# Kernel optimization log

Hardware: AMD Instinct MI355X
Metric: run time of the kernel (lower is better)

The kernel has to match this reference:

```python
import jax, jax.numpy as jnp
import numpy as np

B, DIN, N = 4096, 1024, 1024

def _hard_sigmoid(z):
    # Keras hard_sigmoid: clip(0.2*x + 0.5, 0, 1)
    return jnp.clip(0.2 * z + 0.5, 0.0, 1.0)

def setup_inputs() -> dict:
    key = jax.random.key(0)
    ks = jax.random.split(key, 12)
    s_in = 1.0 / np.sqrt(DIN)
    s_h = 1.0 / np.sqrt(N)
    d = {
        'x': jax.random.normal(ks[0], (B, DIN), jnp.float32),
        'c0': jax.random.normal(ks[1], (B, N), jnp.float32),
        'h0': jax.random.normal(ks[2], (B, N), jnp.float32),
        'Wf': jax.random.normal(ks[3], (DIN, N), jnp.float32) * s_in,
        'Wi': jax.random.normal(ks[4], (DIN, N), jnp.float32) * s_in,
        'Wo': jax.random.normal(ks[5], (DIN, N), jnp.float32) * s_in,
        'Wc': jax.random.normal(ks[6], (DIN, N), jnp.float32) * s_in,
        'Uf': jax.random.normal(ks[7], (N, N), jnp.float32) * s_h,
        'Ui': jax.random.normal(ks[8], (N, N), jnp.float32) * s_h,
        'Uo': jax.random.normal(ks[9], (N, N), jnp.float32) * s_h,
        'Uc': jax.random.normal(ks[10], (N, N), jnp.float32) * s_h,
        'bf': jnp.zeros((N,), jnp.float32),
        'bi': jnp.zeros((N,), jnp.float32),
        'bo': jnp.zeros((N,), jnp.float32),
        'bc': jnp.zeros((N,), jnp.float32),
    }
    return d

def reference(x, c0, h0, Wf, Wi, Wo, Wc, Uf, Ui, Uo, Uc, bf, bi, bo, bc):
    # Fuse the 8 small Dense ops into two GEMMs on concatenated weights
    W = jnp.concatenate([Wf, Wi, Wo, Wc], axis=1)            # [DIN, 4N]
    U = jnp.concatenate([Uf, Ui, Uo, Uc], axis=1)            # [N, 4N]
    b = jnp.concatenate([bf, bi, bo, bc], axis=0)            # [4N]
    z = x @ W + h0 @ U + b                                   # [B, 4N]
    zf, zi, zo, zc = jnp.split(z, 4, axis=1)
    f = _hard_sigmoid(zf)
    i = _hard_sigmoid(zi)
    o = _hard_sigmoid(zo)
    c_tilde = jnp.tanh(zc)
    c = f * c0 + i * c_tilde
    h = o * jnp.tanh(c)
    return (h, c, h)  # (output, new_c, new_h)
```

## Files before the change

kernel.cpp:

```cpp
#include <hip/hip_runtime.h>
#include <hip/hip_bf16.h>
#include <stdint.h>

typedef unsigned short u16;
typedef __attribute__((ext_vector_type(8))) short short8;
typedef __attribute__((ext_vector_type(4))) float f32x4;

#define BATCH 4096
#define DIN   1024
#define NH    1024
#define KTOT  2048
#define BM    128
#define BN    32
#define BK    64

__device__ __forceinline__ void gload_lds16(const void* gp, void* lp) {
    __builtin_amdgcn_global_load_lds(
        (const __attribute__((address_space(1))) uint32_t*)gp,
        (__attribute__((address_space(3))) uint32_t*)lp, 16, 0, 0);
}

__device__ __forceinline__ u16 f2bf(float f) {
    uint32_t t; __builtin_memcpy(&t, &f, 4);
    uint32_t r = (t + 0x7FFFu + ((t >> 16) & 1u)) >> 16;
    return (u16)r;
}
__device__ __forceinline__ float hsig(float z) {
    return fminf(fmaxf(fmaf(z, 0.2f, 0.5f), 0.0f), 1.0f);
}
__device__ __forceinline__ float fast_tanh(float x) {
    x = fminf(fmaxf(x, -12.0f), 12.0f);
    float e = __expf(2.0f * x);
    return (e - 1.0f) / (e + 1.0f);
}

#define WT_BLOCKS 2048
__global__ __launch_bounds__(256) void prep_kernel(
    const float* __restrict__ x, const float* __restrict__ h0,
    const float* __restrict__ Wf, const float* __restrict__ Wi,
    const float* __restrict__ Wo, const float* __restrict__ Wc,
    const float* __restrict__ Uf, const float* __restrict__ Ui,
    const float* __restrict__ Uo, const float* __restrict__ Uc,
    u16* __restrict__ Bt, u16* __restrict__ Abuf)
{
    __shared__ u16 tile[64][65];
    const int bid = blockIdx.x;
    const int tid = threadIdx.x;

    if (bid < WT_BLOCKS) {
        const int mz = bid >> 8;
        const float* srcs[8] = {Wf, Wi, Wo, Wc, Uf, Ui, Uo, Uc};
        const float* src = srcs[mz];
        const int g    = mz & 3;
        const int koff = (mz >> 2) << 10;
        const int k0 = ((bid >> 4) & 15) * 64;
        const int n0 = (bid & 15) * 64;

#pragma unroll
        for (int i = 0; i < 4; i++) {
            int idx = i * 256 + tid;
            int kk = idx >> 4, c = idx & 15;
            float4 v = *(const float4*)(src + (size_t)(k0 + kk) * NH + n0 + c * 4);
            u16* dst = &tile[kk][c * 4];
            dst[0] = f2bf(v.x); dst[1] = f2bf(v.y);
            dst[2] = f2bf(v.z); dst[3] = f2bf(v.w);
        }
        __syncthreads();
#pragma unroll
        for (int i = 0; i < 2; i++) {
            int idx = i * 256 + tid;
            int nn = idx >> 3, c = idx & 7;
            union { u16 v[8]; uint4 q; } pk;
#pragma unroll
            for (int j = 0; j < 8; j++) pk.v[j] = tile[c * 8 + j][nn];
            *(uint4*)(Bt + ((size_t)(g * NH + n0 + nn)) * KTOT + koff + k0 + c * 8) = pk.q;
        }
    } else {
        const int c  = (bid - WT_BLOCKS) * 256 + tid;
        const int m  = c >> 8;
        const int kc = (c & 255) * 8;
        const float* src = (kc < DIN) ? (x + (size_t)m * DIN + kc)
                                      : (h0 + (size_t)m * DIN + (kc - DIN));
        float4 v0 = *(const float4*)(src);
        float4 v1 = *(const float4*)(src + 4);
        union { u16 v[8]; uint4 q; } pk;
        pk.v[0] = f2bf(v0.x); pk.v[1] = f2bf(v0.y);
        pk.v[2] = f2bf(v0.z); pk.v[3] = f2bf(v0.w);
        pk.v[4] = f2bf(v1.x); pk.v[5] = f2bf(v1.y);
        pk.v[6] = f2bf(v1.z); pk.v[7] = f2bf(v1.w);
        *(uint4*)(Abuf + (size_t)m * KTOT + kc) = pk.q;
    }
}

__global__ __launch_bounds__(256, 2) void lstm_gemm_kernel(
    const u16* __restrict__ Abuf, const float* __restrict__ c0,
    const u16* __restrict__ Bt,
    const float* __restrict__ bfv, const float* __restrict__ biv,
    const float* __restrict__ bov, const float* __restrict__ bcv,
    float* __restrict__ out)
{
    __shared__ u16 As[BM * BK];
    __shared__ u16 Bs[4 * BN * BK];

    const int tid  = threadIdx.x;
    const int wv   = tid >> 6;
    const int lane = tid & 63;
    const int m0 = blockIdx.x * BM;
    const int n0 = blockIdx.y * BN;

    const int lr  = lane >> 3;
    const int lcs = ((lane & 7) ^ lr) * 8;

    f32x4 acc[2][4][2];
#pragma unroll
    for (int mt = 0; mt < 2; mt++)
#pragma unroll
        for (int g = 0; g < 4; g++)
#pragma unroll
            for (int nt = 0; nt < 2; nt++)
                acc[mt][g][nt] = (f32x4){0.f, 0.f, 0.f, 0.f};

    const int am   = lane & 15;
    const int am7  = am & 7;
    const int quad = lane >> 4;

    for (int k0 = 0; k0 < KTOT; k0 += BK) {
#pragma unroll
        for (int j = 0; j < 4; j++) {
            int r = (wv * 4 + j) * 8 + lr;
            gload_lds16(Abuf + (size_t)(m0 + r) * KTOT + k0 + lcs,
                        (void*)(As + (wv * 4 + j) * 512));
        }
#pragma unroll
        for (int j = 0; j < 4; j++) {
            int rowIdx = (wv * 4 + j) * 8 + lr;
            int grow = (rowIdx >> 5) * NH + n0 + (rowIdx & 31);
            gload_lds16(Bt + (size_t)grow * KTOT + k0 + lcs,
                        (void*)(Bs + (wv * 4 + j) * 512));
        }
        __syncthreads();
#pragma unroll
        for (int ks = 0; ks < 2; ks++) {
            const int sw = (((ks * 4 + quad) ^ am7) << 3);
            short8 a0 = *(const short8*)(As + (wv * 32 +      am) * BK + sw);
            short8 a1 = *(const short8*)(As + (wv * 32 + 16 + am) * BK + sw);
#pragma unroll
            for (int g = 0; g < 4; g++) {
#pragma unroll
                for (int nt = 0; nt < 2; nt++) {
                    short8 b = *(const short8*)(Bs + (g * 32 + nt * 16 + am) * BK + sw);
                    acc[0][g][nt] = __builtin_amdgcn_mfma_f32_16x16x32_bf16(a0, b, acc[0][g][nt], 0, 0, 0);
                    acc[1][g][nt] = __builtin_amdgcn_mfma_f32_16x16x32_bf16(a1, b, acc[1][g][nt], 0, 0, 0);
                }
            }
        }
        __syncthreads();
    }

    float bias[4][2];
    const float* bptr[4] = {bfv, biv, bov, bcv};
#pragma unroll
    for (int g = 0; g < 4; g++)
#pragma unroll
        for (int nt = 0; nt < 2; nt++)
            bias[g][nt] = bptr[g][n0 + nt * 16 + am];

    const size_t HN = (size_t)BATCH * NH;
#pragma unroll
    for (int mt = 0; mt < 2; mt++) {
#pragma unroll
        for (int r = 0; r < 4; r++) {
            const int row = m0 + wv * 32 + mt * 16 + quad * 4 + r;
#pragma unroll
            for (int nt = 0; nt < 2; nt++) {
                const int col = n0 + nt * 16 + am;
                const size_t off = (size_t)row * NH + col;
                float zf = acc[mt][0][nt][r] + bias[0][nt];
                float zi = acc[mt][1][nt][r] + bias[1][nt];
                float zo = acc[mt][2][nt][r] + bias[2][nt];
                float zc = acc[mt][3][nt][r] + bias[3][nt];
                float fg = hsig(zf), ig = hsig(zi), og = hsig(zo);
                float ct = fast_tanh(zc);
                float cn = fg * c0[off] + ig * ct;
                float hn = og * fast_tanh(cn);
                out[off]            = hn;
                out[HN + off]       = cn;
                out[2 * HN + off]   = hn;
            }
        }
    }
}

extern "C" void kernel_launch(void* const* d_in, const int* in_sizes, int n_in,
                              void* d_out, int out_size, void* d_ws, size_t ws_size,
                              hipStream_t stream) {
    const float* x  = (const float*)d_in[0];
    const float* c0 = (const float*)d_in[1];
    const float* h0 = (const float*)d_in[2];
    const float* Wf = (const float*)d_in[3];
    const float* Wi = (const float*)d_in[4];
    const float* Wo = (const float*)d_in[5];
    const float* Wc = (const float*)d_in[6];
    const float* Uf = (const float*)d_in[7];
    const float* Ui = (const float*)d_in[8];
    const float* Uo = (const float*)d_in[9];
    const float* Uc = (const float*)d_in[10];
    const float* bf = (const float*)d_in[11];
    const float* bi = (const float*)d_in[12];
    const float* bo = (const float*)d_in[13];
    const float* bc = (const float*)d_in[14];

    u16* Bt   = (u16*)d_ws;
    u16* Abuf = (u16*)d_ws + (size_t)4 * NH * KTOT;

    prep_kernel<<<WT_BLOCKS + (BATCH * KTOT / 8) / 256, 256, 0, stream>>>(
        x, h0, Wf, Wi, Wo, Wc, Uf, Ui, Uo, Uc, Bt, Abuf);

    dim3 gg(BATCH / BM, NH / BN);
    lstm_gemm_kernel<<<gg, 256, 0, stream>>>(Abuf, c0, Bt, bf, bi, bo, bc,
                                             (float*)d_out);
}
```

Before: 218.1 us.

## Remap blocks per XCD and reshape per-wave tile to 64x16 per gate

Changes the launch to a 1D grid of 1024 blocks and remaps block ids so that consecutive blocks landing on the same XCD share N-column tiles (four N tiles per XCD), improving L2 reuse of the weight matrix. It also restructures the per-wave work from 32 rows x 32 cols to 64 rows x 16 cols per gate. Each B fragment load now feeds four MFMAs instead of two, and LDS reads per k-step drop from 10 to 8 per wave. The epilogue now handles 16 rows per lane, with one column per lane instead of two, which changes the store pattern. The remap assumes round-robin dispatch of blocks to 8 XCDs.

```diff
diff --git a/kernel.cpp b/kernel.cpp
--- a/kernel.cpp
+++ b/kernel.cpp
@@ -105,20 +105,27 @@
     const int tid  = threadIdx.x;
     const int wv   = tid >> 6;
     const int lane = tid & 63;
-    const int m0 = blockIdx.x * BM;
-    const int n0 = blockIdx.y * BN;
+
+    const int b   = blockIdx.x;
+    const int xcd = b & 7;
+    const int q   = b >> 3;
+    const int by  = xcd * 4 + (q >> 5);
+    const int bx  = q & 31;
+    const int m0 = bx * BM;
+    const int n0 = by * BN;
+
+    const int wr = (wv >> 1) * 64;
+    const int wc = (wv & 1) * 16;
 
     const int lr  = lane >> 3;
     const int lcs = ((lane & 7) ^ lr) * 8;
 
-    f32x4 acc[2][4][2];
-#pragma unroll
-    for (int mt = 0; mt < 2; mt++)
+    f32x4 acc[4][4];
+#pragma unroll
+    for (int mt = 0; mt < 4; mt++)
 #pragma unroll
         for (int g = 0; g < 4; g++)
-#pragma unroll
-            for (int nt = 0; nt < 2; nt++)
-                acc[mt][g][nt] = (f32x4){0.f, 0.f, 0.f, 0.f};
+            acc[mt][g] = (f32x4){0.f, 0.f, 0.f, 0.f};
 
     const int am   = lane & 15;
     const int am7  = am & 7;
@@ -142,51 +149,43 @@
 #pragma unroll
         for (int ks = 0; ks < 2; ks++) {
             const int sw = (((ks * 4 + quad) ^ am7) << 3);
-            short8 a0 = *(const short8*)(As + (wv * 32 +      am) * BK + sw);
-            short8 a1 = *(const short8*)(As + (wv * 32 + 16 + am) * BK + sw);
+            short8 a[4];
+#pragma unroll
+            for (int mt = 0; mt < 4; mt++)
+                a[mt] = *(const short8*)(As + (wr + mt * 16 + am) * BK + sw);
 #pragma unroll
             for (int g = 0; g < 4; g++) {
-#pragma unroll
-                for (int nt = 0; nt < 2; nt++) {
-                    short8 b = *(const short8*)(Bs + (g * 32 + nt * 16 + am) * BK + sw);
-                    acc[0][g][nt] = __builtin_amdgcn_mfma_f32_16x16x32_bf16(a0, b, acc[0][g][nt], 0, 0, 0);
-                    acc[1][g][nt] = __builtin_amdgcn_mfma_f32_16x16x32_bf16(a1, b, acc[1][g][nt], 0, 0, 0);
-                }
+                short8 bfrag = *(const short8*)(Bs + (g * 32 + wc + am) * BK + sw);
+#pragma unroll
+                for (int mt = 0; mt < 4; mt++)
+                    acc[mt][g] = __builtin_amdgcn_mfma_f32_16x16x32_bf16(
+                        a[mt], bfrag, acc[mt][g], 0, 0, 0);
             }
         }
         __syncthreads();
     }
 
-    float bias[4][2];
-    const float* bptr[4] = {bfv, biv, bov, bcv};
-#pragma unroll
-    for (int g = 0; g < 4; g++)
-#pragma unroll
-        for (int nt = 0; nt < 2; nt++)
-            bias[g][nt] = bptr[g][n0 + nt * 16 + am];
+    const int col = n0 + wc + am;
+    float bias0 = bfv[col], bias1 = biv[col], bias2 = bov[col], bias3 = bcv[col];
 
     const size_t HN = (size_t)BATCH * NH;
 #pragma unroll
-    for (int mt = 0; mt < 2; mt++) {
+    for (int mt = 0; mt < 4; mt++) {
 #pragma unroll
         for (int r = 0; r < 4; r++) {
-            const int row = m0 + wv * 32 + mt * 16 + quad * 4 + r;
-#pragma unroll
-            for (int nt = 0; nt < 2; nt++) {
-                const int col = n0 + nt * 16 + am;
-                const size_t off = (size_t)row * NH + col;
-                float zf = acc[mt][0][nt][r] + bias[0][nt];
-                float zi = acc[mt][1][nt][r] + bias[1][nt];
-                float zo = acc[mt][2][nt][r] + bias[2][nt];
-                float zc = acc[mt][3][nt][r] + bias[3][nt];
-                float fg = hsig(zf), ig = hsig(zi), og = hsig(zo);
-                float ct = fast_tanh(zc);
-                float cn = fg * c0[off] + ig * ct;
-                float hn = og * fast_tanh(cn);
-                out[off]            = hn;
-                out[HN + off]       = cn;
-                out[2 * HN + off]   = hn;
-            }
+            const int row = m0 + wr + mt * 16 + quad * 4 + r;
+            const size_t off = (size_t)row * NH + col;
+            float zf = acc[mt][0][r] + bias0;
+            float zi = acc[mt][1][r] + bias1;
+            float zo = acc[mt][2][r] + bias2;
+            float zc = acc[mt][3][r] + bias3;
+            float fg = hsig(zf), ig = hsig(zi), og = hsig(zo);
+            float ct = fast_tanh(zc);
+            float cn = fg * c0[off] + ig * ct;
+            float hn = og * fast_tanh(cn);
+            out[off]            = hn;
+            out[HN + off]       = cn;
+            out[2 * HN + off]   = hn;
         }
     }
 }
@@ -216,7 +215,6 @@
     prep_kernel<<<WT_BLOCKS + (BATCH * KTOT / 8) / 256, 256, 0, stream>>>(
         x, h0, Wf, Wi, Wo, Wc, Uf, Ui, Uo, Uc, Bt, Abuf);
 
-    dim3 gg(BATCH / BM, NH / BN);
-    lstm_gemm_kernel<<<gg, 256, 0, stream>>>(Abuf, c0, Bt, bf, bi, bo, bc,
-                                             (float*)d_out);
-}
+    lstm_gemm_kernel<<<1024, 256, 0, stream>>>(Abuf, c0, Bt, bf, bi, bo, bc,
+                                               (float*)d_out);
+}
```

New measurement: 216.3 us. Within noise of the previous version (-0.8%).
